# Performance work log

Hardware: AMD Instinct MI355X
Metric: run time of the kernel (lower is better)

Reference implementation:

```python
import jax, jax.numpy as jnp
import numpy as np

B, S, D, H = 2, 2048, 1024, 16
DK = D // H  # 64
THETA = 10000.0


def _rope_tables(max_seq_len, d_k, theta):
    dim_idx = jnp.arange(0, d_k // 2, dtype=jnp.float32)
    freqs = 1.0 / theta ** (2.0 * dim_idx / d_k)
    pos = jnp.arange(0, max_seq_len, dtype=jnp.float32)
    ang = jnp.outer(pos, freqs)  # [S, d_k//2]
    return jnp.sin(ang), jnp.cos(ang)


def setup_inputs() -> dict:
    key = jax.random.key(0)
    ks = jax.random.split(key, 5)
    scale = 0.02
    x = jax.random.normal(ks[0], (B, S, D), dtype=jnp.float32)
    w_q = jax.random.normal(ks[1], (D, D), dtype=jnp.float32) * scale
    w_k = jax.random.normal(ks[2], (D, D), dtype=jnp.float32) * scale
    w_v = jax.random.normal(ks[3], (D, D), dtype=jnp.float32) * scale
    w_o = jax.random.normal(ks[4], (D, D), dtype=jnp.float32) * scale
    sin_tab, cos_tab = _rope_tables(S, DK, THETA)
    token_positions = jnp.broadcast_to(jnp.arange(S, dtype=jnp.int32), (B, S))
    return {"x": x, "w_q": w_q, "w_k": w_k, "w_v": w_v, "w_o": w_o,
            "sin_tab": sin_tab, "cos_tab": cos_tab,
            "token_positions": token_positions}


def _apply_rope(t, sin, cos):
    # t: [B, H, S, DK]; sin/cos: [B, 1, S, DK//2]
    t_even = t[..., 0::2]
    t_odd = t[..., 1::2]
    r_even = cos * t_even - sin * t_odd
    r_odd = sin * t_even + cos * t_odd
    # re-interleave even/odd back into last dim
    out = jnp.stack([r_even, r_odd], axis=-1)  # [B,H,S,DK//2,2]
    return out.reshape(t.shape)


def reference(x, w_q, w_k, w_v, w_o, sin_tab, cos_tab, token_positions):
    b, s, d = x.shape
    q = (x @ w_q.T).reshape(b, s, H, DK).transpose(0, 2, 1, 3)  # [B,H,S,DK]
    k = (x @ w_k.T).reshape(b, s, H, DK).transpose(0, 2, 1, 3)
    v = (x @ w_v.T).reshape(b, s, H, DK).transpose(0, 2, 1, 3)

    sin = sin_tab[token_positions][:, None, :, :]  # [B,1,S,DK//2]
    cos = cos_tab[token_positions][:, None, :, :]
    q = _apply_rope(q, sin, cos)
    k = _apply_rope(k, sin, cos)

    scores = jnp.einsum('bhqd,bhkd->bhqk', q, k) / jnp.sqrt(jnp.float32(DK))
    causal = jnp.tril(jnp.ones((s, s), dtype=bool))  # keep lower triangle
    scores = jnp.where(causal, scores, -jnp.inf)
    probs = jax.nn.softmax(scores, axis=-1)
    attn = jnp.einsum('bhqk,bhkd->bhqd', probs, v)
    attn = attn.transpose(0, 2, 1, 3).reshape(b, s, d)
    return attn @ w_o.T
```

## Files before the change

kernel.cpp:

```cpp
#include <hip/hip_runtime.h>
#include <hip/hip_bf16.h>
#include <cstdint>

#define B_ 2
#define S_ 2048
#define D_ 1024
#define H_ 16
#define DK_ 64
#define HALF_ 32

typedef short bf16x8 __attribute__((ext_vector_type(8)));
typedef float f32x4  __attribute__((ext_vector_type(4)));
typedef unsigned int u32;

static __device__ __forceinline__ unsigned short bfbits(float f) {
    __hip_bfloat16 h = __float2bfloat16(f);
    unsigned short u; __builtin_memcpy(&u, &h, 2); return u;
}
static __device__ __forceinline__ unsigned pack2bf(float a, float b) {
    return (unsigned)bfbits(a) | ((unsigned)bfbits(b) << 16);
}

static __device__ __forceinline__ void gload_lds16(const void* g, void* l) {
    __builtin_amdgcn_global_load_lds(
        (const __attribute__((address_space(1))) u32*)(uintptr_t)g,
        (__attribute__((address_space(3))) u32*)(uintptr_t)l,
        16, 0, 0);
}

__global__ __launch_bounds__(256) void to_bf16_kernel(
    const float* __restrict__ x,
    const float* __restrict__ wq, const float* __restrict__ wk,
    const float* __restrict__ wv, const float* __restrict__ wo,
    const float* __restrict__ sin_tab, const float* __restrict__ cos_tab,
    __hip_bfloat16* __restrict__ xb,
    __hip_bfloat16* __restrict__ wqb, __hip_bfloat16* __restrict__ wkb,
    __hip_bfloat16* __restrict__ wvb, __hip_bfloat16* __restrict__ wob,
    float2* __restrict__ sctab)
{
    const int seg = blockIdx.y;
    if (seg == 8) {
        if (blockIdx.x >= 64) return;
        size_t i = ((size_t)blockIdx.x * 256 + threadIdx.x) * 4;
        float4 c = *reinterpret_cast<const float4*>(cos_tab + i);
        float4 s = *reinterpret_cast<const float4*>(sin_tab + i);
        float4* dst = reinterpret_cast<float4*>(sctab + i);
        dst[0] = make_float4(c.x, s.x, c.y, s.y);
        dst[1] = make_float4(c.z, s.z, c.w, s.w);
        return;
    }
    const float* src;
    __hip_bfloat16* dst;
    size_t off = 0;
    if (seg < 4)       { src = x;  dst = xb;  off = (size_t)seg << 20; }
    else if (seg == 4) { src = wq; dst = wqb; }
    else if (seg == 5) { src = wk; dst = wkb; }
    else if (seg == 6) { src = wv; dst = wvb; }
    else               { src = wo; dst = wob; }
    size_t i = off + ((size_t)blockIdx.x * 256 + threadIdx.x) * 4;
    float4 v = *reinterpret_cast<const float4*>(src + i);
    ushort4 u = make_ushort4(bfbits(v.x), bfbits(v.y), bfbits(v.z), bfbits(v.w));
    *reinterpret_cast<ushort4*>(dst + i) = u;
}

template<int MODE>
__global__ __launch_bounds__(256) void mfma_gemm_kernel(
    const __hip_bfloat16* __restrict__ A,
    const __hip_bfloat16* __restrict__ Wq, const __hip_bfloat16* __restrict__ Wk,
    const __hip_bfloat16* __restrict__ Wv,
    __hip_bfloat16* __restrict__ out_q, __hip_bfloat16* __restrict__ out_k,
    __hip_bfloat16* __restrict__ out_v,
    float* __restrict__ out_f32,
    const float2* __restrict__ sctab,
    const int* __restrict__ tpos)
{
    constexpr int K = 1024;
    const int which = (MODE == 0) ? blockIdx.z : 3;
    const __hip_bfloat16* __restrict__ W =
        (MODE == 1) ? Wq : (which == 0 ? Wq : which == 1 ? Wk : Wv);

    __shared__ __align__(16) unsigned char As[2][128 * 4 * 16];
    __shared__ __align__(16) unsigned char Bs[2][128 * 4 * 16];

    const int tid = threadIdx.x;
    const int wid = tid >> 6;
    const int l   = tid & 63;
    const int g   = l >> 4;
    const int i16 = l & 15;
    const int wr  = wid >> 1, wc = wid & 1;

    const int wg   = blockIdx.x;
    const int tile = (wg & 7) * 32 + (wg >> 3);
    const int row0 = (tile >> 3) * 128;
    const int col0 = (tile & 7) * 128;

    const __hip_bfloat16* Abase = A + (size_t)row0 * K;
    const __hip_bfloat16* Wbase = W + (size_t)col0 * K;

    f32x4 acc[4][4];
    const f32x4 zero = {0.f, 0.f, 0.f, 0.f};
    #pragma unroll
    for (int mi = 0; mi < 4; ++mi)
        #pragma unroll
        for (int ni = 0; ni < 4; ++ni) acc[mi][ni] = zero;

    int a_off[4], b_off[4];
    #pragma unroll
    for (int f = 0; f < 4; ++f) {
        int ra = wr * 64 + f * 16 + i16;
        a_off[f] = (ra * 4 + (g ^ ((ra >> 1) & 3))) * 16;
        int rb = wc * 64 + f * 16 + i16;
        b_off[f] = (rb * 4 + (g ^ ((rb >> 1) & 3))) * 16;
    }

    int st_goff[2], st_loff[2];
    #pragma unroll
    for (int it = 0; it < 2; ++it) {
        int c = it * 256 + wid * 64 + l;
        int row = c >> 2;
        int kc = (c & 3) ^ ((row >> 1) & 3);
        st_goff[it] = row * K + kc * 8;
        st_loff[it] = (it * 256 + wid * 64) * 16;
    }

    #pragma unroll
    for (int it = 0; it < 2; ++it) {
        gload_lds16(Abase + st_goff[it], &As[0][0] + st_loff[it]);
        gload_lds16(Wbase + st_goff[it], &Bs[0][0] + st_loff[it]);
    }
    __syncthreads();

    for (int t = 0; t < K / 32; ++t) {
        const int cur = t & 1;
        if (t + 1 < K / 32) {
            const int k1 = (t + 1) * 32;
            #pragma unroll
            for (int it = 0; it < 2; ++it) {
                gload_lds16(Abase + k1 + st_goff[it], &As[cur ^ 1][0] + st_loff[it]);
                gload_lds16(Wbase + k1 + st_goff[it], &Bs[cur ^ 1][0] + st_loff[it]);
            }
        }
        bf16x8 af[4], bfr[4];
        #pragma unroll
        for (int f = 0; f < 4; ++f) {
            af[f]  = *reinterpret_cast<const bf16x8*>(&As[cur][0] + a_off[f]);
            bfr[f] = *reinterpret_cast<const bf16x8*>(&Bs[cur][0] + b_off[f]);
        }
        #pragma unroll
        for (int mi = 0; mi < 4; ++mi)
            #pragma unroll
            for (int ni = 0; ni < 4; ++ni)
                acc[mi][ni] = __builtin_amdgcn_mfma_f32_16x16x32_bf16(
                    af[mi], bfr[ni], acc[mi][ni], 0, 0, 0);
        __syncthreads();
    }

    if (MODE == 0) {
        __hip_bfloat16* __restrict__ outp =
            which == 0 ? out_q : which == 1 ? out_k : out_v;
        const int head = (col0 >> 6) + wc;
        #pragma unroll
        for (int mi = 0; mi < 4; ++mi) {
            #pragma unroll
            for (int r = 0; r < 4; ++r) {
                const int gi = row0 + wr * 64 + mi * 16 + g * 4 + r;
                const int b_ = gi >> 11;
                const int s_ = gi & (S_ - 1);
                const int pos = tpos[gi];
                const float2* sc = sctab + pos * HALF_;
                __hip_bfloat16* orow =
                    outp + (((size_t)b_ * H_ + head) * S_ + s_) * DK_;
                #pragma unroll
                for (int ni = 0; ni < 4; ++ni) {
                    float val = acc[mi][ni][r];
                    float other = __shfl_xor(val, 1, 64);
                    const int dk = ni * 16 + i16;
                    float res;
                    if (which < 2) {
                        float2 cs = sc[ni * 8 + (i16 >> 1)];
                        res = (i16 & 1) ? fmaf(cs.y, other, cs.x * val)
                                        : (cs.x * val - cs.y * other);
                    } else {
                        res = val;
                    }
                    if (which == 0) res *= 0.125f;
                    orow[dk] = __float2bfloat16(res);
                }
            }
        }
    } else {
        #pragma unroll
        for (int mi = 0; mi < 4; ++mi) {
            #pragma unroll
            for (int r = 0; r < 4; ++r) {
                const int gi = row0 + wr * 64 + mi * 16 + g * 4 + r;
                float* orow = out_f32 + (size_t)gi * D_ + col0 + wc * 64;
                #pragma unroll
                for (int ni = 0; ni < 4; ++ni)
                    orow[ni * 16 + i16] = acc[mi][ni][r];
            }
        }
    }
}

__global__ __launch_bounds__(512) void flash_mfma_kernel(
    const __hip_bfloat16* __restrict__ q,
    const __hip_bfloat16* __restrict__ k,
    const __hip_bfloat16* __restrict__ v,
    __hip_bfloat16* __restrict__ attn)
{
    __shared__ __align__(16) unsigned char Ks[2][64 * 128];
    __shared__ __align__(16) unsigned char Vt[2][64 * 128];
    __shared__ __align__(16) unsigned char Ps[8][16 * 128];

    const int tid = threadIdx.x;
    const int w   = tid >> 6;
    const int l   = tid & 63;
    const int g   = l >> 4;
    const int i16 = l & 15;
    const int pid = blockIdx.x;
    const int bh  = blockIdx.y;
    const size_t base = (size_t)bh * S_ * DK_;
    const __hip_bfloat16* kb_ = k + base;
    const __hip_bfloat16* vb_ = v + base;

    const int ci     = w * 64 + l;
    const int krow   = ci >> 3;
    const int kchunk = (ci & 7) ^ (krow & 7);
    const int ksrc   = krow * DK_ + kchunk * 8;
    unsigned char* const pw = &Ps[w][0];

    for (int pp = 0; pp < 2; ++pp) {
        const int qsb   = pp ? (15 - pid) : pid;
        const int qrow  = qsb * 128 + w * 16 + i16;
        const int qbase = qsb * 128 + w * 16;
        const int nt    = 2 * qsb + 2;

        bf16x8 qf0, qf1;
        {
            const __hip_bfloat16* qp = q + base + (size_t)qrow * DK_ + g * 8;
            qf0 = *reinterpret_cast<const bf16x8*>(qp);
            qf1 = *reinterpret_cast<const bf16x8*>(qp + 32);
        }

        f32x4 o[4] = {};
        float m_run = -1e30f, l_run = 0.0f;

        gload_lds16(kb_ + ksrc, &Ks[0][0] + w * 1024);
        {
            float4 vv = *reinterpret_cast<const float4*>(vb_ + l * DK_ + w * 8);
            const unsigned short* u = reinterpret_cast<const unsigned short*>(&vv);
            #pragma unroll
            for (int s = 0; s < 8; ++s) {
                int d = w * 8 + s;
                *reinterpret_cast<unsigned short*>(&Vt[0][0] + d * 128 +
                    (((l >> 3) ^ (d & 7)) << 4) + (l & 7) * 2) = u[s];
            }
        }
        __syncthreads();

        for (int t = 0; t < nt; ++t) {
            const int cur = t & 1;
            const bool pre = (t + 1 < nt);
            float4 vv;
            if (pre) {
                gload_lds16(kb_ + (size_t)(t + 1) * 64 * DK_ + ksrc,
                            &Ks[cur ^ 1][0] + w * 1024);
                vv = *reinterpret_cast<const float4*>(
                    vb_ + (size_t)(t + 1) * 64 * DK_ + l * DK_ + w * 8);
            }

            if (t * 64 <= qbase + 15) {
                f32x4 s_acc[4] = {};
                __builtin_amdgcn_s_setprio(1);
                #pragma unroll
                for (int jf = 0; jf < 4; ++jf) {
                    int row = jf * 16 + i16;
                    bf16x8 ak0 = *reinterpret_cast<const bf16x8*>(
                        &Ks[cur][0] + row * 128 + ((g ^ (row & 7)) << 4));
                    s_acc[jf] = __builtin_amdgcn_mfma_f32_16x16x32_bf16(
                        ak0, qf0, s_acc[jf], 0, 0, 0);
                    bf16x8 ak1 = *reinterpret_cast<const bf16x8*>(
                        &Ks[cur][0] + row * 128 + (((4 + g) ^ (row & 7)) << 4));
                    s_acc[jf] = __builtin_amdgcn_mfma_f32_16x16x32_bf16(
                        ak1, qf1, s_acc[jf], 0, 0, 0);
                }
                __builtin_amdgcn_s_setprio(0);

                if (t * 64 + 63 > qbase) {
                    #pragma unroll
                    for (int jf = 0; jf < 4; ++jf)
                        #pragma unroll
                        for (int r = 0; r < 4; ++r)
                            if (t * 64 + jf * 16 + g * 4 + r > qrow)
                                s_acc[jf][r] = -1e30f;
                }

                float vmax = -1e30f;
                #pragma unroll
                for (int jf = 0; jf < 4; ++jf)
                    #pragma unroll
                    for (int r = 0; r < 4; ++r)
                        vmax = fmaxf(vmax, s_acc[jf][r]);
                vmax = fmaxf(vmax, __shfl_xor(vmax, 16, 64));
                vmax = fmaxf(vmax, __shfl_xor(vmax, 32, 64));
                float m_new = fmaxf(m_run, vmax);
                float factor = __expf(m_run - m_new);
                m_run = m_new;

                float p[4][4];
                float psum = 0.0f;
                #pragma unroll
                for (int jf = 0; jf < 4; ++jf)
                    #pragma unroll
                    for (int r = 0; r < 4; ++r) {
                        p[jf][r] = __expf(s_acc[jf][r] - m_new);
                        psum += p[jf][r];
                    }
                psum += __shfl_xor(psum, 16, 64);
                psum += __shfl_xor(psum, 32, 64);
                l_run = l_run * factor + psum;
                #pragma unroll
                for (int df = 0; df < 4; ++df)
                    #pragma unroll
                    for (int r = 0; r < 4; ++r)
                        o[df][r] *= factor;

                #pragma unroll
                for (int jf = 0; jf < 4; ++jf)
                    #pragma unroll
                    for (int r0 = 0; r0 < 4; r0 += 2) {
                        unsigned pk = pack2bf(p[jf][r0], p[jf][r0 + 1]);
                        int jj = jf * 16 + g * 4 + r0;
                        *reinterpret_cast<unsigned*>(pw + i16 * 128 +
                            ((jj * 2) ^ ((i16 & 7) << 4))) = pk;
                    }

                __builtin_amdgcn_s_setprio(1);
                #pragma unroll
                for (int jc = 0; jc < 2; ++jc) {
                    bf16x8 bp = *reinterpret_cast<const bf16x8*>(pw + i16 * 128 +
                        (((jc * 4 + g) ^ (i16 & 7)) << 4));
                    #pragma unroll
                    for (int df = 0; df < 4; ++df) {
                        int row = df * 16 + i16;
                        bf16x8 av = *reinterpret_cast<const bf16x8*>(
                            &Vt[cur][0] + row * 128 +
                            (((jc * 4 + g) ^ (row & 7)) << 4));
                        o[df] = __builtin_amdgcn_mfma_f32_16x16x32_bf16(
                            av, bp, o[df], 0, 0, 0);
                    }
                }
                __builtin_amdgcn_s_setprio(0);
            }

            if (pre) {
                const unsigned short* u = reinterpret_cast<const unsigned short*>(&vv);
                unsigned char* vtb = &Vt[cur ^ 1][0];
                #pragma unroll
                for (int s = 0; s < 8; ++s) {
                    int d = w * 8 + s;
                    *reinterpret_cast<unsigned short*>(vtb + d * 128 +
                        (((l >> 3) ^ (d & 7)) << 4) + (l & 7) * 2) = u[s];
                }
            }
            __syncthreads();
        }

        const float inv_l = 1.0f / l_run;
        const int b_ = bh >> 4, h_ = bh & 15;
        __hip_bfloat16* orow = attn + ((size_t)b_ * S_ + qrow) * D_ + h_ * 64;
        #pragma unroll
        for (int df = 0; df < 4; ++df) {
            ushort4 uo = make_ushort4(
                bfbits(o[df][0] * inv_l), bfbits(o[df][1] * inv_l),
                bfbits(o[df][2] * inv_l), bfbits(o[df][3] * inv_l));
            *reinterpret_cast<ushort4*>(orow + df * 16 + g * 4) = uo;
        }
    }
}

extern "C" void kernel_launch(void* const* d_in, const int* in_sizes, int n_in,
                              void* d_out, int out_size, void* d_ws, size_t ws_size,
                              hipStream_t stream) {
    const float* x       = (const float*)d_in[0];
    const float* w_q     = (const float*)d_in[1];
    const float* w_k     = (const float*)d_in[2];
    const float* w_v     = (const float*)d_in[3];
    const float* w_o     = (const float*)d_in[4];
    const float* sin_tab = (const float*)d_in[5];
    const float* cos_tab = (const float*)d_in[6];
    const int*   tpos    = (const int*)d_in[7];
    float* out = (float*)d_out;

    const size_t nM  = (size_t)B_ * S_ * D_;
    const size_t nW  = (size_t)D_ * D_;
    __hip_bfloat16* xb   = (__hip_bfloat16*)d_ws;
    __hip_bfloat16* wqb  = xb  + nM;
    __hip_bfloat16* wkb  = wqb + nW;
    __hip_bfloat16* wvb  = wkb + nW;
    __hip_bfloat16* wob  = wvb + nW;
    __hip_bfloat16* q_ws = wob + nW;
    __hip_bfloat16* k_ws = q_ws + nM;
    __hip_bfloat16* v_ws = k_ws + nM;
    __hip_bfloat16* a_ws = v_ws + nM;
    float2*         sct  = (float2*)(a_ws + nM);

    to_bf16_kernel<<<dim3(1024, 9), 256, 0, stream>>>(
        x, w_q, w_k, w_v, w_o, sin_tab, cos_tab,
        xb, wqb, wkb, wvb, wob, sct);
    mfma_gemm_kernel<0><<<dim3(256, 1, 3), 256, 0, stream>>>(
        xb, wqb, wkb, wvb, q_ws, k_ws, v_ws, nullptr, sct, tpos);
    flash_mfma_kernel<<<dim3(8, B_ * H_), 512, 0, stream>>>(
        q_ws, k_ws, v_ws, a_ws);
    mfma_gemm_kernel<1><<<dim3(256, 1, 1), 256, 0, stream>>>(
        a_ws, wob, nullptr, nullptr, nullptr, nullptr, nullptr, out,
        sct, tpos);
}
```

Baseline: 140.0 us.

## Split flash attention into one block per Q tile, use exp2 and lazy rescaling

The attention kernel now launches one workgroup per (batch-head, 128-row query tile), 512 in total, instead of 256 workgroups that each process a paired short and long query tile. Tiles are ordered so the longest causal tiles are scheduled first, with heads interleaved across blocks. The softmax scale is folded into Q as 1/sqrt(dk)·log2(e), so exp2 replaces expf. The running-max rescale of O and l is skipped when the new max exceeds the old by at most 11.5, which cuts per-tile VALU work. The cost is a dependence on the longest-first ordering to balance load, plus a bounded growth of intermediate exponentials that could reduce precision.

```diff
diff --git a/kernel.cpp b/kernel.cpp
--- a/kernel.cpp
+++ b/kernel.cpp
@@ -183,7 +183,7 @@
                     } else {
                         res = val;
                     }
-                    if (which == 0) res *= 0.125f;
+                    if (which == 0) res *= 0.180336880f;
                     orow[dk] = __float2bfloat16(res);
                 }
             }
@@ -218,8 +218,11 @@
     const int l   = tid & 63;
     const int g   = l >> 4;
     const int i16 = l & 15;
-    const int pid = blockIdx.x;
-    const int bh  = blockIdx.y;
+
+    const int wgid = blockIdx.x;
+    const int bh   = (wgid & 7) * 4 + ((wgid >> 3) & 3);
+    const int qsb  = 15 - (wgid >> 5);
+
     const size_t base = (size_t)bh * S_ * DK_;
     const __hip_bfloat16* kb_ = k + base;
     const __hip_bfloat16* vb_ = v + base;
@@ -230,153 +233,157 @@
     const int ksrc   = krow * DK_ + kchunk * 8;
     unsigned char* const pw = &Ps[w][0];
 
-    for (int pp = 0; pp < 2; ++pp) {
-        const int qsb   = pp ? (15 - pid) : pid;
-        const int qrow  = qsb * 128 + w * 16 + i16;
-        const int qbase = qsb * 128 + w * 16;
-        const int nt    = 2 * qsb + 2;
-
-        bf16x8 qf0, qf1;
-        {
-            const __hip_bfloat16* qp = q + base + (size_t)qrow * DK_ + g * 8;
-            qf0 = *reinterpret_cast<const bf16x8*>(qp);
-            qf1 = *reinterpret_cast<const bf16x8*>(qp + 32);
-        }
-
-        f32x4 o[4] = {};
-        float m_run = -1e30f, l_run = 0.0f;
-
-        gload_lds16(kb_ + ksrc, &Ks[0][0] + w * 1024);
-        {
-            float4 vv = *reinterpret_cast<const float4*>(vb_ + l * DK_ + w * 8);
-            const unsigned short* u = reinterpret_cast<const unsigned short*>(&vv);
-            #pragma unroll
-            for (int s = 0; s < 8; ++s) {
-                int d = w * 8 + s;
-                *reinterpret_cast<unsigned short*>(&Vt[0][0] + d * 128 +
-                    (((l >> 3) ^ (d & 7)) << 4) + (l & 7) * 2) = u[s];
-            }
-        }
-        __syncthreads();
-
-        for (int t = 0; t < nt; ++t) {
-            const int cur = t & 1;
-            const bool pre = (t + 1 < nt);
-            float4 vv;
-            if (pre) {
-                gload_lds16(kb_ + (size_t)(t + 1) * 64 * DK_ + ksrc,
-                            &Ks[cur ^ 1][0] + w * 1024);
-                vv = *reinterpret_cast<const float4*>(
-                    vb_ + (size_t)(t + 1) * 64 * DK_ + l * DK_ + w * 8);
-            }
-
-            if (t * 64 <= qbase + 15) {
-                f32x4 s_acc[4] = {};
-                __builtin_amdgcn_s_setprio(1);
-                #pragma unroll
-                for (int jf = 0; jf < 4; ++jf) {
-                    int row = jf * 16 + i16;
-                    bf16x8 ak0 = *reinterpret_cast<const bf16x8*>(
-                        &Ks[cur][0] + row * 128 + ((g ^ (row & 7)) << 4));
-                    s_acc[jf] = __builtin_amdgcn_mfma_f32_16x16x32_bf16(
-                        ak0, qf0, s_acc[jf], 0, 0, 0);
-                    bf16x8 ak1 = *reinterpret_cast<const bf16x8*>(
-                        &Ks[cur][0] + row * 128 + (((4 + g) ^ (row & 7)) << 4));
-                    s_acc[jf] = __builtin_amdgcn_mfma_f32_16x16x32_bf16(
-                        ak1, qf1, s_acc[jf], 0, 0, 0);
-                }
-                __builtin_amdgcn_s_setprio(0);
-
-                if (t * 64 + 63 > qbase) {
-                    #pragma unroll
-                    for (int jf = 0; jf < 4; ++jf)
-                        #pragma unroll
-                        for (int r = 0; r < 4; ++r)
-                            if (t * 64 + jf * 16 + g * 4 + r > qrow)
-                                s_acc[jf][r] = -1e30f;
-                }
-
-                float vmax = -1e30f;
+    const int qrow  = qsb * 128 + w * 16 + i16;
+    const int qbase = qsb * 128 + w * 16;
+    const int nt    = 2 * qsb + 2;
+
+    bf16x8 qf0, qf1;
+    {
+        const __hip_bfloat16* qp = q + base + (size_t)qrow * DK_ + g * 8;
+        qf0 = *reinterpret_cast<const bf16x8*>(qp);
+        qf1 = *reinterpret_cast<const bf16x8*>(qp + 32);
+    }
+
+    f32x4 o[4] = {};
+    float m_run = -1e30f, l_run = 0.0f;
+
+    gload_lds16(kb_ + ksrc, &Ks[0][0] + w * 1024);
+    {
+        float4 vv = *reinterpret_cast<const float4*>(vb_ + l * DK_ + w * 8);
+        const unsigned short* u = reinterpret_cast<const unsigned short*>(&vv);
+        #pragma unroll
+        for (int s = 0; s < 8; ++s) {
+            int d = w * 8 + s;
+            *reinterpret_cast<unsigned short*>(&Vt[0][0] + d * 128 +
+                (((l >> 3) ^ (d & 7)) << 4) + (l & 7) * 2) = u[s];
+        }
+    }
+    __syncthreads();
+
+    for (int t = 0; t < nt; ++t) {
+        const int cur = t & 1;
+        const bool pre = (t + 1 < nt);
+        float4 vv;
+        if (pre) {
+            gload_lds16(kb_ + (size_t)(t + 1) * 64 * DK_ + ksrc,
+                        &Ks[cur ^ 1][0] + w * 1024);
+            vv = *reinterpret_cast<const float4*>(
+                vb_ + (size_t)(t + 1) * 64 * DK_ + l * DK_ + w * 8);
+        }
+
+        if (t * 64 <= qbase + 15) {
+            f32x4 s_acc[4] = {};
+            __builtin_amdgcn_s_setprio(1);
+            #pragma unroll
+            for (int jf = 0; jf < 4; ++jf) {
+                int row = jf * 16 + i16;
+                bf16x8 ak0 = *reinterpret_cast<const bf16x8*>(
+                    &Ks[cur][0] + row * 128 + ((g ^ (row & 7)) << 4));
+                s_acc[jf] = __builtin_amdgcn_mfma_f32_16x16x32_bf16(
+                    ak0, qf0, s_acc[jf], 0, 0, 0);
+                bf16x8 ak1 = *reinterpret_cast<const bf16x8*>(
+                    &Ks[cur][0] + row * 128 + (((4 + g) ^ (row & 7)) << 4));
+                s_acc[jf] = __builtin_amdgcn_mfma_f32_16x16x32_bf16(
+                    ak1, qf1, s_acc[jf], 0, 0, 0);
+            }
+            __builtin_amdgcn_s_setprio(0);
+
+            if (t * 64 + 63 > qbase) {
                 #pragma unroll
                 for (int jf = 0; jf < 4; ++jf)
                     #pragma unroll
                     for (int r = 0; r < 4; ++r)
-                        vmax = fmaxf(vmax, s_acc[jf][r]);
-                vmax = fmaxf(vmax, __shfl_xor(vmax, 16, 64));
-                vmax = fmaxf(vmax, __shfl_xor(vmax, 32, 64));
+                        if (t * 64 + jf * 16 + g * 4 + r > qrow)
+                            s_acc[jf][r] = -1e30f;
+            }
+
+            float mx01 = fmaxf(fmaxf(s_acc[0][0], s_acc[0][1]),
+                               fmaxf(s_acc[0][2], s_acc[0][3]));
+            float mx02 = fmaxf(fmaxf(s_acc[1][0], s_acc[1][1]),
+                               fmaxf(s_acc[1][2], s_acc[1][3]));
+            float mx03 = fmaxf(fmaxf(s_acc[2][0], s_acc[2][1]),
+                               fmaxf(s_acc[2][2], s_acc[2][3]));
+            float mx04 = fmaxf(fmaxf(s_acc[3][0], s_acc[3][1]),
+                               fmaxf(s_acc[3][2], s_acc[3][3]));
+            float vmax = fmaxf(fmaxf(mx01, mx02), fmaxf(mx03, mx04));
+            vmax = fmaxf(vmax, __shfl_xor(vmax, 16, 64));
+            vmax = fmaxf(vmax, __shfl_xor(vmax, 32, 64));
+
+            if (!__all(vmax <= m_run + 11.5f)) {
                 float m_new = fmaxf(m_run, vmax);
-                float factor = __expf(m_run - m_new);
+                float factor = __builtin_amdgcn_exp2f(m_run - m_new);
                 m_run = m_new;
-
-                float p[4][4];
-                float psum = 0.0f;
-                #pragma unroll
-                for (int jf = 0; jf < 4; ++jf)
-                    #pragma unroll
-                    for (int r = 0; r < 4; ++r) {
-                        p[jf][r] = __expf(s_acc[jf][r] - m_new);
-                        psum += p[jf][r];
-                    }
-                psum += __shfl_xor(psum, 16, 64);
-                psum += __shfl_xor(psum, 32, 64);
-                l_run = l_run * factor + psum;
+                l_run *= factor;
                 #pragma unroll
                 for (int df = 0; df < 4; ++df)
                     #pragma unroll
                     for (int r = 0; r < 4; ++r)
                         o[df][r] *= factor;
-
-                #pragma unroll
-                for (int jf = 0; jf < 4; ++jf)
-                    #pragma unroll
-                    for (int r0 = 0; r0 < 4; r0 += 2) {
-                        unsigned pk = pack2bf(p[jf][r0], p[jf][r0 + 1]);
-                        int jj = jf * 16 + g * 4 + r0;
-                        *reinterpret_cast<unsigned*>(pw + i16 * 128 +
-                            ((jj * 2) ^ ((i16 & 7) << 4))) = pk;
-                    }
-
-                __builtin_amdgcn_s_setprio(1);
-                #pragma unroll
-                for (int jc = 0; jc < 2; ++jc) {
-                    bf16x8 bp = *reinterpret_cast<const bf16x8*>(pw + i16 * 128 +
-                        (((jc * 4 + g) ^ (i16 & 7)) << 4));
-                    #pragma unroll
-                    for (int df = 0; df < 4; ++df) {
-                        int row = df * 16 + i16;
-                        bf16x8 av = *reinterpret_cast<const bf16x8*>(
-                            &Vt[cur][0] + row * 128 +
-                            (((jc * 4 + g) ^ (row & 7)) << 4));
-                        o[df] = __builtin_amdgcn_mfma_f32_16x16x32_bf16(
-                            av, bp, o[df], 0, 0, 0);
-                    }
+            }
+
+            float p[4][4];
+            float psum = 0.0f;
+            #pragma unroll
+            for (int jf = 0; jf < 4; ++jf)
+                #pragma unroll
+                for (int r = 0; r < 4; ++r) {
+                    p[jf][r] = __builtin_amdgcn_exp2f(s_acc[jf][r] - m_run);
+                    psum += p[jf][r];
                 }
-                __builtin_amdgcn_s_setprio(0);
-            }
-
-            if (pre) {
-                const unsigned short* u = reinterpret_cast<const unsigned short*>(&vv);
-                unsigned char* vtb = &Vt[cur ^ 1][0];
-                #pragma unroll
-                for (int s = 0; s < 8; ++s) {
-                    int d = w * 8 + s;
-                    *reinterpret_cast<unsigned short*>(vtb + d * 128 +
-                        (((l >> 3) ^ (d & 7)) << 4) + (l & 7) * 2) = u[s];
+            psum += __shfl_xor(psum, 16, 64);
+            psum += __shfl_xor(psum, 32, 64);
+            l_run += psum;
+
+            #pragma unroll
+            for (int jf = 0; jf < 4; ++jf)
+                #pragma unroll
+                for (int r0 = 0; r0 < 4; r0 += 2) {
+                    unsigned pk = pack2bf(p[jf][r0], p[jf][r0 + 1]);
+                    int jj = jf * 16 + g * 4 + r0;
+                    *reinterpret_cast<unsigned*>(pw + i16 * 128 +
+                        ((jj * 2) ^ ((i16 & 7) << 4))) = pk;
                 }
-            }
-            __syncthreads();
-        }
-
-        const float inv_l = 1.0f / l_run;
-        const int b_ = bh >> 4, h_ = bh & 15;
-        __hip_bfloat16* orow = attn + ((size_t)b_ * S_ + qrow) * D_ + h_ * 64;
-        #pragma unroll
-        for (int df = 0; df < 4; ++df) {
-            ushort4 uo = make_ushort4(
-                bfbits(o[df][0] * inv_l), bfbits(o[df][1] * inv_l),
-                bfbits(o[df][2] * inv_l), bfbits(o[df][3] * inv_l));
-            *reinterpret_cast<ushort4*>(orow + df * 16 + g * 4) = uo;
-        }
+
+            __builtin_amdgcn_s_setprio(1);
+            #pragma unroll
+            for (int jc = 0; jc < 2; ++jc) {
+                bf16x8 bp = *reinterpret_cast<const bf16x8*>(pw + i16 * 128 +
+                    (((jc * 4 + g) ^ (i16 & 7)) << 4));
+                #pragma unroll
+                for (int df = 0; df < 4; ++df) {
+                    int row = df * 16 + i16;
+                    bf16x8 av = *reinterpret_cast<const bf16x8*>(
+                        &Vt[cur][0] + row * 128 +
+                        (((jc * 4 + g) ^ (row & 7)) << 4));
+                    o[df] = __builtin_amdgcn_mfma_f32_16x16x32_bf16(
+                        av, bp, o[df], 0, 0, 0);
+                }
+            }
+            __builtin_amdgcn_s_setprio(0);
+        }
+
+        if (pre) {
+            const unsigned short* u = reinterpret_cast<const unsigned short*>(&vv);
+            unsigned char* vtb = &Vt[cur ^ 1][0];
+            #pragma unroll
+            for (int s = 0; s < 8; ++s) {
+                int d = w * 8 + s;
+                *reinterpret_cast<unsigned short*>(vtb + d * 128 +
+                    (((l >> 3) ^ (d & 7)) << 4) + (l & 7) * 2) = u[s];
+            }
+        }
+        __syncthreads();
+    }
+
+    const float inv_l = 1.0f / l_run;
+    const int b_ = bh >> 4, h_ = bh & 15;
+    __hip_bfloat16* orow = attn + ((size_t)b_ * S_ + qrow) * D_ + h_ * 64;
+    #pragma unroll
+    for (int df = 0; df < 4; ++df) {
+        ushort4 uo = make_ushort4(
+            bfbits(o[df][0] * inv_l), bfbits(o[df][1] * inv_l),
+            bfbits(o[df][2] * inv_l), bfbits(o[df][3] * inv_l));
+        *reinterpret_cast<ushort4*>(orow + df * 16 + g * 4) = uo;
     }
 }
 
@@ -411,7 +418,7 @@
         xb, wqb, wkb, wvb, wob, sct);
     mfma_gemm_kernel<0><<<dim3(256, 1, 3), 256, 0, stream>>>(
         xb, wqb, wkb, wvb, q_ws, k_ws, v_ws, nullptr, sct, tpos);
-    flash_mfma_kernel<<<dim3(8, B_ * H_), 512, 0, stream>>>(
+    flash_mfma_kernel<<<512, 512, 0, stream>>>(
         q_ws, k_ws, v_ws, a_ws);
     mfma_gemm_kernel<1><<<dim3(256, 1, 1), 256, 0, stream>>>(
         a_ws, wob, nullptr, nullptr, nullptr, nullptr, nullptr, out,
```

Result: faster. 132.4 us (-5.4%).
